# Optimization experiments

Measured on AMD Instinct MI355X. Metric: run time of the kernel, lower is better.

Reference implementation:

```python
import jax, jax.numpy as jnp
import numpy as np

N_NODES = 50000
N_EDGES = 800000
IN_CH = 128
OUT_CH = 64
HEADS = 1
NEG_SLOPE = 0.2

def _glorot(key, shape):
    stdv = np.sqrt(6.0 / (shape[-2] + shape[-1]))
    return jax.random.uniform(key, shape, jnp.float32, -stdv, stdv)

def setup_inputs() -> dict:
    key = jax.random.key(0)
    k1, k2, k3, k4, k5 = jax.random.split(key, 5)
    x = jax.random.normal(k1, (N_NODES, IN_CH), jnp.float32)
    src = jax.random.randint(k2, (N_EDGES,), 0, N_NODES)
    dst = jax.random.randint(k3, (N_EDGES,), 0, N_NODES)
    # ensure no pre-existing self loops (remove_self_loops is then identity)
    dst = jnp.where(src == dst, (dst + 1) % N_NODES, dst)
    edge_index = jnp.stack([src, dst]).astype(jnp.int64)
    weight = _glorot(k4, (IN_CH, HEADS * OUT_CH))
    att = _glorot(k5, (1, HEADS, 2 * OUT_CH))
    bias = jnp.zeros((OUT_CH,), jnp.float32)
    return {"x": x, "edge_index": edge_index, "weight": weight, "att": att, "bias": bias}

def reference(x, edge_index, weight, att, bias):
    N = x.shape[0]
    # linear projection -> [N, heads, out]
    h = (x @ weight).reshape(N, HEADS, OUT_CH)
    # add self loops (input guaranteed free of self loops)
    loops = jnp.arange(N, dtype=edge_index.dtype)
    src = jnp.concatenate([edge_index[0], loops])  # source j
    dst = jnp.concatenate([edge_index[1], loops])  # target i
    x_j = h[src]   # [E+N, heads, out]
    x_i = h[dst]
    # attention logits: (cat([x_i, x_j]) * att).sum(-1) -> [E+N, heads]
    alpha = jnp.concatenate([x_i, x_j], axis=-1)
    alpha = (alpha * att).sum(axis=-1)
    alpha = jax.nn.leaky_relu(alpha, NEG_SLOPE)
    # segment softmax over destination nodes
    amax = jax.ops.segment_max(alpha, dst, num_segments=N)
    e = jnp.exp(alpha - amax[dst])
    esum = jax.ops.segment_sum(e, dst, num_segments=N)
    alpha = e / (esum[dst] + 1e-16)
    # message + scatter-add aggregation
    msg = x_j * alpha[:, :, None]
    out = jax.ops.segment_sum(msg, dst, num_segments=N)  # [N, heads, out]
    out = out.mean(axis=1) + bias
    # F.normalize (L2, dim=1, eps=1e-12); dropout is eval-mode identity
    norm = jnp.maximum(jnp.linalg.norm(out, axis=1, keepdims=True), 1e-12)
    return out / norm
```

## Files before the change

kernel.cpp:

```cpp
#include <hip/hip_runtime.h>
#include <math.h>

#define IN_CH 128
#define OUT_CH 64
#define NEG_SLOPE 0.2f

__device__ __forceinline__ unsigned short f2bf(float f) {
    unsigned u = __float_as_uint(f);
    unsigned r = (u + 0x7FFFu + ((u >> 16) & 1u)) >> 16;
    return (unsigned short)r;
}

__device__ __forceinline__ bool sniff_is64(const void* edges) {
    const unsigned* up = (const unsigned*)edges;
    bool is64 = true;
#pragma unroll
    for (int k = 0; k < 16; k++) is64 = is64 && (up[2 * k + 1] == 0u);
    return is64;
}

__global__ void k_init(int* counts, int N) {
    int i = blockIdx.x * blockDim.x + threadIdx.x;
    if (i < N) counts[i] = 0;
}

__global__ __launch_bounds__(256) void k_mm_count(
        const float* __restrict__ x, const float* __restrict__ W,
        const float* __restrict__ att, unsigned short* __restrict__ h16,
        float* __restrict__ asrc, float* __restrict__ adst, int N,
        const void* __restrict__ edges, int* __restrict__ counts,
        unsigned short* __restrict__ rank, int E, int mmb) {
    __shared__ float Ws[IN_CH * OUT_CH];
    int t = threadIdx.x;
    if ((int)blockIdx.x >= mmb) {
        int e0 = ((blockIdx.x - mmb) * 256 + t) * 2;
        if (e0 >= E) return;
        bool has1 = (e0 + 1 < E);
        int d0, d1 = 0;
        if (sniff_is64(edges)) {
            const long long* p = (const long long*)edges;
            int4 v = *(const int4*)&p[(size_t)E + e0];
            d0 = v.x; d1 = v.z;
        } else {
            const int* p = (const int*)edges;
            int2 v = *(const int2*)&p[E + e0];
            d0 = v.x; d1 = v.y;
        }
        rank[e0] = (unsigned short)atomicAdd(counts + d0, 1);
        if (has1) rank[e0 + 1] = (unsigned short)atomicAdd(counts + d1, 1);
        return;
    }
    for (int i = t * 4; i < IN_CH * OUT_CH; i += 256 * 4)
        *(float4*)&Ws[i] = *(const float4*)&W[i];
    int cg = t & 15, g = t >> 4;
    float4 att_d = *(const float4*)&att[cg * 4];
    float4 att_s = *(const float4*)&att[64 + cg * 4];
    __syncthreads();

    int n0 = blockIdx.x * 64 + g * 4;
    int nn[4];
#pragma unroll
    for (int m = 0; m < 4; m++) nn[m] = min(n0 + m, N - 1);

    float4 acc[4];
#pragma unroll
    for (int m = 0; m < 4; m++) acc[m] = make_float4(0.f, 0.f, 0.f, 0.f);

#pragma unroll 2
    for (int k4 = 0; k4 < IN_CH / 4; k4++) {
        float4 xv[4];
#pragma unroll
        for (int m = 0; m < 4; m++)
            xv[m] = *(const float4*)&x[(size_t)nn[m] * IN_CH + k4 * 4];
        float4 wv[4];
#pragma unroll
        for (int j = 0; j < 4; j++)
            wv[j] = *(const float4*)&Ws[(k4 * 4 + j) * OUT_CH + cg * 4];
#pragma unroll
        for (int m = 0; m < 4; m++) {
            acc[m].x = fmaf(xv[m].x, wv[0].x, acc[m].x);
            acc[m].y = fmaf(xv[m].x, wv[0].y, acc[m].y);
            acc[m].z = fmaf(xv[m].x, wv[0].z, acc[m].z);
            acc[m].w = fmaf(xv[m].x, wv[0].w, acc[m].w);
            acc[m].x = fmaf(xv[m].y, wv[1].x, acc[m].x);
            acc[m].y = fmaf(xv[m].y, wv[1].y, acc[m].y);
            acc[m].z = fmaf(xv[m].y, wv[1].z, acc[m].z);
            acc[m].w = fmaf(xv[m].y, wv[1].w, acc[m].w);
            acc[m].x = fmaf(xv[m].z, wv[2].x, acc[m].x);
            acc[m].y = fmaf(xv[m].z, wv[2].y, acc[m].y);
            acc[m].z = fmaf(xv[m].z, wv[2].z, acc[m].z);
            acc[m].w = fmaf(xv[m].z, wv[2].w, acc[m].w);
            acc[m].x = fmaf(xv[m].w, wv[3].x, acc[m].x);
            acc[m].y = fmaf(xv[m].w, wv[3].y, acc[m].y);
            acc[m].z = fmaf(xv[m].w, wv[3].z, acc[m].z);
            acc[m].w = fmaf(xv[m].w, wv[3].w, acc[m].w);
        }
    }

#pragma unroll
    for (int m = 0; m < 4; m++) {
        int node = n0 + m;
        if (node < N) {
            ushort4 hv;
            hv.x = f2bf(acc[m].x);
            hv.y = f2bf(acc[m].y);
            hv.z = f2bf(acc[m].z);
            hv.w = f2bf(acc[m].w);
            *(ushort4*)&h16[(size_t)node * OUT_CH + cg * 4] = hv;
        }
        float pd = acc[m].x * att_d.x + acc[m].y * att_d.y +
                   acc[m].z * att_d.z + acc[m].w * att_d.w;
        float ps = acc[m].x * att_s.x + acc[m].y * att_s.y +
                   acc[m].z * att_s.z + acc[m].w * att_s.w;
#pragma unroll
        for (int msk = 1; msk < 16; msk <<= 1) {
            pd += __shfl_xor(pd, msk, 64);
            ps += __shfl_xor(ps, msk, 64);
        }
        if (cg == 0 && node < N) { adst[node] = pd; asrc[node] = ps; }
    }
}

__global__ __launch_bounds__(256) void k_scanA(const int* __restrict__ counts,
                                               int* __restrict__ partials, int N) {
    __shared__ int red[256];
    int t = threadIdx.x;
    int base = blockIdx.x * 1024 + t * 4;
    int s = 0;
    if (base + 3 < N) {
        int4 v = *(const int4*)(counts + base);
        s = v.x + v.y + v.z + v.w;
    } else {
        for (int i = 0; i < 4; i++) if (base + i < N) s += counts[base + i];
    }
    red[t] = s;
    __syncthreads();
    for (int off = 128; off > 0; off >>= 1) {
        if (t < off) red[t] += red[t + off];
        __syncthreads();
    }
    if (t == 0) partials[blockIdx.x] = red[0];
}

__global__ __launch_bounds__(256) void k_scanC(const int* __restrict__ counts,
                                               const int* __restrict__ partials,
                                               int nb, int total,
                                               int* __restrict__ rowptr, int N) {
    __shared__ int shp[256];
    __shared__ int sh[256];
    int t = threadIdx.x;
    shp[t] = (t < nb) ? partials[t] : 0;
    __syncthreads();
    for (int off = 1; off < 256; off <<= 1) {
        int v = (t >= off) ? shp[t - off] : 0;
        __syncthreads();
        shp[t] += v;
        __syncthreads();
    }
    int base_blk = (blockIdx.x == 0) ? 0 : shp[blockIdx.x - 1];

    int base = blockIdx.x * 1024 + t * 4;
    int c[4];
    int s = 0;
#pragma unroll
    for (int i = 0; i < 4; i++) {
        int idx = base + i;
        c[i] = (idx < N) ? counts[idx] : 0;
        s += c[i];
    }
    sh[t] = s;
    __syncthreads();
    for (int off = 1; off < 256; off <<= 1) {
        int v = (t >= off) ? sh[t - off] : 0;
        __syncthreads();
        sh[t] += v;
        __syncthreads();
    }
    int run = ((t == 0) ? 0 : sh[t - 1]) + base_blk;
#pragma unroll
    for (int i = 0; i < 4; i++) {
        int idx = base + i;
        if (idx < N) {
            rowptr[idx] = run;
            run += c[i];
        }
    }
    if (blockIdx.x == 0 && t == 0) rowptr[N] = total;
}

__global__ void k_scatter(const void* __restrict__ edges,
                          const unsigned short* __restrict__ rank,
                          const int* __restrict__ rowptr,
                          int* __restrict__ csr_src, int E) {
    int e0 = (blockIdx.x * blockDim.x + threadIdx.x) * 2;
    if (e0 >= E) return;
    bool has1 = (e0 + 1 < E);
    int s0, s1 = 0, d0, d1 = 0;
    if (sniff_is64(edges)) {
        const long long* p = (const long long*)edges;
        int4 vs = *(const int4*)&p[e0];
        int4 vd = *(const int4*)&p[(size_t)E + e0];
        s0 = vs.x; s1 = vs.z;
        d0 = vd.x; d1 = vd.z;
    } else {
        const int* p = (const int*)edges;
        int2 vs = *(const int2*)&p[e0];
        int2 vd = *(const int2*)&p[E + e0];
        s0 = vs.x; s1 = vs.y;
        d0 = vd.x; d1 = vd.y;
    }
    ushort2 r = *(const ushort2*)&rank[e0];
    csr_src[rowptr[d0] + r.x] = s0;
    if (has1) csr_src[rowptr[d1] + r.y] = s1;
}

__global__ __launch_bounds__(256) void k_agg(const unsigned short* __restrict__ h16,
                                             const int* __restrict__ csr_src,
                                             const int* __restrict__ rowptr,
                                             const float* __restrict__ asrc,
                                             const float* __restrict__ adst,
                                             const float* __restrict__ bias,
                                             float* __restrict__ out, int N) {
    __shared__ float2 stage[4][64];
    int lane = threadIdx.x & 63;
    int wid = threadIdx.x >> 6;
    int node = blockIdx.x * 4 + wid;
    if (node >= N) return;
    int half = lane >> 5;
    int ch2 = (lane & 31) * 2;

    float aD = adst[node];
    float a = aD + asrc[node];
    a = a > 0.f ? a : NEG_SLOPE * a;
    float w_self = __expf(a);
    unsigned hv = *(const unsigned*)&h16[(size_t)node * OUT_CH + ch2];
    float wse = half ? 0.f : w_self;
    float accx = wse * __uint_as_float(hv << 16);
    float accy = wse * __uint_as_float(hv & 0xFFFF0000u);
    float esum_lane = 0.f;

    int b0 = rowptr[node], b1 = rowptr[node + 1];
    for (int base = b0; base < b1; base += 64) {
        int idx = base + lane;
        int sv = 0;
        float wv = 0.f;
        if (idx < b1) {
            sv = csr_src[idx];
            float av = aD + asrc[sv];
            av = av > 0.f ? av : NEG_SLOPE * av;
            wv = __expf(av);
        }
        esum_lane += wv;
        stage[wid][lane] = make_float2(__int_as_float(sv), wv);

        int n = min(64, b1 - base);
        for (int j = 0; j < n; j += 8) {
#pragma unroll
            for (int k = 0; k < 4; k++) {
                float2 p = stage[wid][j + 2 * k + half];
                int s = __float_as_int(p.x);
                unsigned v = *(const unsigned*)&h16[((size_t)s << 6) + ch2];
                accx = fmaf(p.y, __uint_as_float(v << 16), accx);
                accy = fmaf(p.y, __uint_as_float(v & 0xFFFF0000u), accy);
            }
        }
    }
    accx += __shfl_xor(accx, 32, 64);
    accy += __shfl_xor(accy, 32, 64);
#pragma unroll
    for (int m = 32; m >= 1; m >>= 1) esum_lane += __shfl_xor(esum_lane, m, 64);
    float esum = esum_lane + w_self;

    float inv = 1.f / (esum + 1e-16f);
    float2 bv = *(const float2*)&bias[ch2];
    float vx = accx * inv + bv.x;
    float vy = accy * inv + bv.y;
    float ss = vx * vx + vy * vy;
#pragma unroll
    for (int m = 16; m >= 1; m >>= 1) ss += __shfl_xor(ss, m, 64);
    float rinv = 1.f / fmaxf(sqrtf(ss), 1e-12f);
    if (!half)
        *(float2*)&out[(size_t)node * OUT_CH + ch2] = make_float2(vx * rinv, vy * rinv);
}

extern "C" void kernel_launch(void* const* d_in, const int* in_sizes, int n_in,
                              void* d_out, int out_size, void* d_ws, size_t ws_size,
                              hipStream_t stream) {
    const float* x    = (const float*)d_in[0];
    const void*  edges = d_in[1];
    const float* W    = (const float*)d_in[2];
    const float* att  = (const float*)d_in[3];
    const float* bias = (const float*)d_in[4];
    float* out = (float*)d_out;

    const int N = in_sizes[0] / IN_CH;
    const int E = in_sizes[1] / 2;
    const int NB = (N + 1023) / 1024;
    const int MMB = (N + 63) / 64;
    const int CNTB = ((E + 1) / 2 + 255) / 256;

    char* ws = (char*)d_ws;
    size_t off = 0;
    auto alloc = [&](size_t bytes) -> void* {
        void* p = ws + off;
        off += bytes;
        off = (off + 255) & ~(size_t)255;
        return p;
    };
    int*            counts   = (int*)alloc((size_t)N * 4);
    int*            rowptr   = (int*)alloc((size_t)(N + 1) * 4);
    unsigned short* rank     = (unsigned short*)alloc((size_t)E * 2);
    int*            partials = (int*)alloc((size_t)256 * 4);
    unsigned short* h16      = (unsigned short*)alloc((size_t)N * OUT_CH * 2);
    float*          asrc     = (float*)alloc((size_t)N * 4);
    float*          adst     = (float*)alloc((size_t)N * 4);
    int*            csr_src  = (int*)alloc((size_t)E * 4);

    k_init<<<(N + 255) / 256, 256, 0, stream>>>(counts, N);
    k_mm_count<<<MMB + CNTB, 256, 0, stream>>>(x, W, att, h16, asrc, adst, N,
                                               edges, counts, rank, E, MMB);
    k_scanA<<<NB, 256, 0, stream>>>(counts, partials, N);
    k_scanC<<<NB, 256, 0, stream>>>(counts, partials, NB, E, rowptr, N);
    k_scatter<<<((E + 1) / 2 + 255) / 256, 256, 0, stream>>>(edges, rank, rowptr,
                                                             csr_src, E);
    k_agg<<<(N + 3) / 4, 256, 0, stream>>>(h16, csr_src, rowptr, asrc, adst,
                                           bias, out, N);
}
```

Measured before the change: 165.7 us.

## Interleave matmul and count blocks, widen edge processing to 4 per thread

The fused matmul+count kernel now interleaves matmul and edge-count blocks by block index, so both roles are scheduled concurrently instead of all count blocks running after the matmul blocks. Count and scatter kernels handle four edges per thread with wider vector loads and ushort4 rank stores. The aggregation inner loop is unrolled further, and the zeroing kernel is replaced with hipMemsetAsync. This aims to cut launch count, index-load overhead and tail imbalance, at the cost of more tail-handling code and higher register use.

```diff
diff --git a/kernel.cpp b/kernel.cpp
--- a/kernel.cpp
+++ b/kernel.cpp
@@ -17,11 +17,6 @@
 #pragma unroll
     for (int k = 0; k < 16; k++) is64 = is64 && (up[2 * k + 1] == 0u);
     return is64;
-}
-
-__global__ void k_init(int* counts, int N) {
-    int i = blockIdx.x * blockDim.x + threadIdx.x;
-    if (i < N) counts[i] = 0;
 }
 
 __global__ __launch_bounds__(256) void k_mm_count(
@@ -29,27 +24,54 @@
         const float* __restrict__ att, unsigned short* __restrict__ h16,
         float* __restrict__ asrc, float* __restrict__ adst, int N,
         const void* __restrict__ edges, int* __restrict__ counts,
-        unsigned short* __restrict__ rank, int E, int mmb) {
+        unsigned short* __restrict__ rank, int E, int mmb, int cntb) {
     __shared__ float Ws[IN_CH * OUT_CH];
     int t = threadIdx.x;
-    if ((int)blockIdx.x >= mmb) {
-        int e0 = ((blockIdx.x - mmb) * 256 + t) * 2;
+    int bid = blockIdx.x;
+    int lo = min(mmb, cntb), M2 = 2 * lo;
+    int role, id;
+    if (bid < M2) { role = bid & 1; id = bid >> 1; }
+    else          { role = (mmb > cntb) ? 0 : 1; id = bid - M2 + lo; }
+
+    if (role == 1) {
+        int e0 = (id * 256 + t) * 4;
         if (e0 >= E) return;
-        bool has1 = (e0 + 1 < E);
-        int d0, d1 = 0;
+        int d[4];
         if (sniff_is64(edges)) {
             const long long* p = (const long long*)edges;
-            int4 v = *(const int4*)&p[(size_t)E + e0];
-            d0 = v.x; d1 = v.z;
+            if (e0 + 3 < E) {
+                int4 v0 = *(const int4*)&p[(size_t)E + e0];
+                int4 v1 = *(const int4*)&p[(size_t)E + e0 + 2];
+                d[0] = v0.x; d[1] = v0.z; d[2] = v1.x; d[3] = v1.z;
+            } else {
+                for (int i = 0; i < 4; i++)
+                    d[i] = (e0 + i < E) ? (int)p[(size_t)E + e0 + i] : 0;
+            }
         } else {
             const int* p = (const int*)edges;
-            int2 v = *(const int2*)&p[E + e0];
-            d0 = v.x; d1 = v.y;
-        }
-        rank[e0] = (unsigned short)atomicAdd(counts + d0, 1);
-        if (has1) rank[e0 + 1] = (unsigned short)atomicAdd(counts + d1, 1);
+            if (e0 + 3 < E) {
+                int4 v = *(const int4*)&p[E + e0];
+                d[0] = v.x; d[1] = v.y; d[2] = v.z; d[3] = v.w;
+            } else {
+                for (int i = 0; i < 4; i++)
+                    d[i] = (e0 + i < E) ? p[E + e0 + i] : 0;
+            }
+        }
+        if (e0 + 3 < E) {
+            ushort4 r;
+            r.x = (unsigned short)atomicAdd(counts + d[0], 1);
+            r.y = (unsigned short)atomicAdd(counts + d[1], 1);
+            r.z = (unsigned short)atomicAdd(counts + d[2], 1);
+            r.w = (unsigned short)atomicAdd(counts + d[3], 1);
+            *(ushort4*)&rank[e0] = r;
+        } else {
+            for (int i = 0; i < 4; i++)
+                if (e0 + i < E)
+                    rank[e0 + i] = (unsigned short)atomicAdd(counts + d[i], 1);
+        }
         return;
     }
+
     for (int i = t * 4; i < IN_CH * OUT_CH; i += 256 * 4)
         *(float4*)&Ws[i] = *(const float4*)&W[i];
     int cg = t & 15, g = t >> 4;
@@ -57,7 +79,7 @@
     float4 att_s = *(const float4*)&att[64 + cg * 4];
     __syncthreads();
 
-    int n0 = blockIdx.x * 64 + g * 4;
+    int n0 = id * 64 + g * 4;
     int nn[4];
 #pragma unroll
     for (int m = 0; m < 4; m++) nn[m] = min(n0 + m, N - 1);
@@ -192,26 +214,47 @@
                           const unsigned short* __restrict__ rank,
                           const int* __restrict__ rowptr,
                           int* __restrict__ csr_src, int E) {
-    int e0 = (blockIdx.x * blockDim.x + threadIdx.x) * 2;
+    int e0 = (blockIdx.x * blockDim.x + threadIdx.x) * 4;
     if (e0 >= E) return;
-    bool has1 = (e0 + 1 < E);
-    int s0, s1 = 0, d0, d1 = 0;
-    if (sniff_is64(edges)) {
-        const long long* p = (const long long*)edges;
-        int4 vs = *(const int4*)&p[e0];
-        int4 vd = *(const int4*)&p[(size_t)E + e0];
-        s0 = vs.x; s1 = vs.z;
-        d0 = vd.x; d1 = vd.z;
+    int s[4], d[4];
+    if (e0 + 3 < E) {
+        if (sniff_is64(edges)) {
+            const long long* p = (const long long*)edges;
+            int4 a0 = *(const int4*)&p[e0];
+            int4 a1 = *(const int4*)&p[e0 + 2];
+            int4 b0 = *(const int4*)&p[(size_t)E + e0];
+            int4 b1 = *(const int4*)&p[(size_t)E + e0 + 2];
+            s[0] = a0.x; s[1] = a0.z; s[2] = a1.x; s[3] = a1.z;
+            d[0] = b0.x; d[1] = b0.z; d[2] = b1.x; d[3] = b1.z;
+        } else {
+            const int* p = (const int*)edges;
+            int4 a = *(const int4*)&p[e0];
+            int4 b = *(const int4*)&p[E + e0];
+            s[0] = a.x; s[1] = a.y; s[2] = a.z; s[3] = a.w;
+            d[0] = b.x; d[1] = b.y; d[2] = b.z; d[3] = b.w;
+        }
+        ushort4 r = *(const ushort4*)&rank[e0];
+        csr_src[rowptr[d[0]] + r.x] = s[0];
+        csr_src[rowptr[d[1]] + r.y] = s[1];
+        csr_src[rowptr[d[2]] + r.z] = s[2];
+        csr_src[rowptr[d[3]] + r.w] = s[3];
     } else {
-        const int* p = (const int*)edges;
-        int2 vs = *(const int2*)&p[e0];
-        int2 vd = *(const int2*)&p[E + e0];
-        s0 = vs.x; s1 = vs.y;
-        d0 = vd.x; d1 = vd.y;
-    }
-    ushort2 r = *(const ushort2*)&rank[e0];
-    csr_src[rowptr[d0] + r.x] = s0;
-    if (has1) csr_src[rowptr[d1] + r.y] = s1;
+        bool is64 = sniff_is64(edges);
+        for (int i = 0; i < 4; i++) {
+            if (e0 + i >= E) break;
+            int sv, dv;
+            if (is64) {
+                const long long* p = (const long long*)edges;
+                sv = (int)p[e0 + i];
+                dv = (int)p[(size_t)E + e0 + i];
+            } else {
+                const int* p = (const int*)edges;
+                sv = p[e0 + i];
+                dv = p[E + e0 + i];
+            }
+            csr_src[rowptr[dv] + rank[e0 + i]] = sv;
+        }
+    }
 }
 
 __global__ __launch_bounds__(256) void k_agg(const unsigned short* __restrict__ h16,
@@ -254,9 +297,9 @@
         stage[wid][lane] = make_float2(__int_as_float(sv), wv);
 
         int n = min(64, b1 - base);
-        for (int j = 0; j < n; j += 8) {
-#pragma unroll
-            for (int k = 0; k < 4; k++) {
+        for (int j = 0; j < n; j += 16) {
+#pragma unroll
+            for (int k = 0; k < 8; k++) {
                 float2 p = stage[wid][j + 2 * k + half];
                 int s = __float_as_int(p.x);
                 unsigned v = *(const unsigned*)&h16[((size_t)s << 6) + ch2];
@@ -297,7 +340,7 @@
     const int E = in_sizes[1] / 2;
     const int NB = (N + 1023) / 1024;
     const int MMB = (N + 63) / 64;
-    const int CNTB = ((E + 1) / 2 + 255) / 256;
+    const int CNTB = (E + 1023) / 1024;
 
     char* ws = (char*)d_ws;
     size_t off = 0;
@@ -316,13 +359,13 @@
     float*          adst     = (float*)alloc((size_t)N * 4);
     int*            csr_src  = (int*)alloc((size_t)E * 4);
 
-    k_init<<<(N + 255) / 256, 256, 0, stream>>>(counts, N);
+    hipMemsetAsync(counts, 0, (size_t)N * 4, stream);
     k_mm_count<<<MMB + CNTB, 256, 0, stream>>>(x, W, att, h16, asrc, adst, N,
-                                               edges, counts, rank, E, MMB);
+                                               edges, counts, rank, E, MMB, CNTB);
     k_scanA<<<NB, 256, 0, stream>>>(counts, partials, N);
     k_scanC<<<NB, 256, 0, stream>>>(counts, partials, NB, E, rowptr, N);
-    k_scatter<<<((E + 1) / 2 + 255) / 256, 256, 0, stream>>>(edges, rank, rowptr,
-                                                             csr_src, E);
+    k_scatter<<<(E + 1023) / 1024, 256, 0, stream>>>(edges, rank, rowptr,
+                                                     csr_src, E);
     k_agg<<<(N + 3) / 4, 256, 0, stream>>>(h16, csr_src, rowptr, asrc, adst,
                                            bias, out, N);
 }
```

Result: faster. 160.2 us (-3.3%).
